# Kernel optimization log

Hardware: AMD Instinct MI355X
Metric: run time of the kernel (lower is better)

Reference implementation:

```python
import jax, jax.numpy as jnp
import numpy as np

N = 100000   # nodes
E = 1600000  # edges (before self loops)
IN, HID, OUT = 128, 128, 64


def setup_inputs() -> dict:
    key = jax.random.key(0)
    ks = jax.random.split(key, 5)
    x = jax.random.normal(ks[0], (N, IN), dtype=jnp.float32)
    edge_index = jax.random.randint(ks[1], (2, E), 0, N, dtype=jnp.int32)
    W1 = jax.random.normal(ks[2], (IN, HID), dtype=jnp.float32) * (1.0 / np.sqrt(IN))
    b1 = jnp.zeros((HID,), dtype=jnp.float32)
    W2 = jax.random.normal(ks[3], (HID, OUT), dtype=jnp.float32) * (1.0 / np.sqrt(HID))
    b2 = jnp.zeros((OUT,), dtype=jnp.float32)
    return {"x": x, "edge_index": edge_index, "W1": W1, "b1": b1, "W2": W2, "b2": b2}


def _gcn_conv(x, W, b, src, dst, norm):
    # linear transform first (small GEMM), then normalized scatter-add aggregation
    h = x @ W                                   # [N, d_out]
    msg = h[src] * norm[:, None]                # [E+N, d_out] gathered messages
    agg = jax.ops.segment_sum(msg, dst, num_segments=N)
    return agg + b


def reference(x, edge_index, W1, b1, W2, b2):
    loops = jnp.arange(N, dtype=edge_index.dtype)
    src = jnp.concatenate([edge_index[0], loops])   # add self loops (PyG GCNConv default)
    dst = jnp.concatenate([edge_index[1], loops])
    # symmetric normalization D^{-1/2} (A+I) D^{-1/2}
    deg = jax.ops.segment_sum(jnp.ones_like(dst, dtype=x.dtype), dst, num_segments=N)
    dinv = jnp.where(deg > 0, jax.lax.rsqrt(deg), 0.0)
    norm = dinv[src] * dinv[dst]                # [E+N]

    h = _gcn_conv(x, W1, b1, src, dst, norm)
    h = jax.nn.relu(h)
    out = _gcn_conv(h, W2, b2, src, dst, norm)
    return out
```

## Files before the change

kernel.cpp:

```cpp
#include <hip/hip_runtime.h>
#include <hip/hip_bf16.h>

#define IN_DIM  128
#define HID_DIM 128
#define OUT_DIM 64
#define NREP    8

typedef unsigned short ushort_t;
struct ushort4_t { ushort_t x, y, z, w; };
typedef __attribute__((ext_vector_type(8))) short bf16x8;
typedef __attribute__((ext_vector_type(4))) float f32x4;

__device__ __forceinline__ float bf2f(ushort_t u) {
    return __uint_as_float(((unsigned int)u) << 16);
}
__device__ __forceinline__ short f2bf_s(float v) {
    __hip_bfloat16 t = __float2bfloat16(v);
    return *(short*)&t;
}
__device__ __forceinline__ unsigned int pack2(float a, float b) {
    return ((unsigned int)(ushort_t)f2bf_s(b) << 16) | (ushort_t)f2bf_s(a);
}

__global__ void count_rank(const int* __restrict__ dst, int E, int N,
                           int* __restrict__ cntR, int* __restrict__ rank) {
    int e = blockIdx.x * blockDim.x + threadIdx.x;
    if (e < E) {
        int r = (e >> 8) & (NREP - 1);
        rank[e] = atomicAdd(&cntR[(size_t)r * N + dst[e]], 1);
    }
}

__global__ void node_totals(int* __restrict__ cntR, float* __restrict__ dinv,
                            int* __restrict__ cntp, int* __restrict__ bsum, int N) {
    __shared__ int wsum[4];
    const int t = threadIdx.x;
    const int base = blockIdx.x * 2048 + t * 8;
    int ssum = 0;
    #pragma unroll
    for (int i = 0; i < 8; ++i) {
        const int idx = base + i;
        if (idx < N) {
            int b = 0;
            #pragma unroll
            for (int r = 0; r < NREP; ++r) {
                int c = cntR[(size_t)r * N + idx];
                cntR[(size_t)r * N + idx] = b;
                b += c;
            }
            dinv[idx] = rsqrtf((float)(b + 1));
            int p = (b + 7) & ~7;
            cntp[idx] = p;
            ssum += p;
        }
    }
    #pragma unroll
    for (int off = 32; off > 0; off >>= 1) ssum += __shfl_down(ssum, off);
    const int lane = t & 63, w = t >> 6;
    if (lane == 0) wsum[w] = ssum;
    __syncthreads();
    if (t == 0) bsum[blockIdx.x] = wsum[0] + wsum[1] + wsum[2] + wsum[3];
}

__global__ void scan_partials(int* __restrict__ bsum, int S) {
    const int t = threadIdx.x;
    int running = 0;
    for (int base = 0; base < S; base += 64) {
        int i = base + t;
        int v = (i < S) ? bsum[i] : 0;
        int incl = v;
        #pragma unroll
        for (int off = 1; off < 64; off <<= 1) {
            int u = __shfl_up(incl, off);
            if (t >= off) incl += u;
        }
        if (i < S) bsum[i] = running + incl - v;
        running += __shfl(incl, 63);
    }
}

__global__ void scan_write(const int* __restrict__ cntp, const int* __restrict__ bsum,
                           int* __restrict__ row_start, int N) {
    __shared__ int wsum[4];
    const int t = threadIdx.x;
    const int base = blockIdx.x * 2048 + t * 8;
    int v[8];
    #pragma unroll
    for (int i = 0; i < 8; ++i) v[i] = (base + i < N) ? cntp[base + i] : 0;
    int s = v[0] + v[1] + v[2] + v[3] + v[4] + v[5] + v[6] + v[7];
    const int lane = t & 63, w = t >> 6;
    int incl = s;
    #pragma unroll
    for (int off = 1; off < 64; off <<= 1) {
        int u = __shfl_up(incl, off);
        if (lane >= off) incl += u;
    }
    if (lane == 63) wsum[w] = incl;
    __syncthreads();
    int woff = 0;
    for (int i = 0; i < w; ++i) woff += wsum[i];
    int run = bsum[blockIdx.x] + woff + (incl - s);
    #pragma unroll
    for (int i = 0; i < 8; ++i) {
        if (base + i < N) row_start[base + i] = run;
        run += v[i];
    }
}

__global__ void fill_pack(const int* __restrict__ src, const int* __restrict__ dst,
                          const int* __restrict__ rank, const int* __restrict__ row_start,
                          const int* __restrict__ cntR, const float* __restrict__ dinv,
                          int E, int N, int2* __restrict__ pack) {
    int e = blockIdx.x * blockDim.x + threadIdx.x;
    if (e < E) {
        int s = src[e], d = dst[e];
        int r = (e >> 8) & (NREP - 1);
        int pos = row_start[d] + cntR[(size_t)r * N + d] + rank[e];
        int2 p;
        p.x = s;
        p.y = __float_as_int(dinv[s] * dinv[d]);
        pack[pos] = p;
    }
}

__global__ __launch_bounds__(256, 2) void gemm1_mfma(
        const float* __restrict__ x, const float* __restrict__ W,
        unsigned int* __restrict__ h, int N, int NT, int NW) {
    const int tid  = threadIdx.x;
    const int lane = tid & 63;
    const int m    = lane & 15;
    const int quad = lane >> 4;
    const int gw   = blockIdx.x * 4 + (tid >> 6);

    bf16x8 a[8][4];
    #pragma unroll
    for (int ct = 0; ct < 8; ++ct)
        #pragma unroll
        for (int kc = 0; kc < 4; ++kc)
            #pragma unroll
            for (int j = 0; j < 8; ++j)
                a[ct][kc][j] = f2bf_s(W[(size_t)(kc * 32 + quad * 8 + j) * HID_DIM + ct * 16 + m]);

    for (int t = gw; t < NT; t += NW) {
        const int n0 = t * 16;
        int node = n0 + m; if (node >= N) node = N - 1;
        const float* xr = x + (size_t)node * IN_DIM + quad * 8;
        f32x4 acc[8];
        #pragma unroll
        for (int ct = 0; ct < 8; ++ct) acc[ct] = (f32x4){0.f, 0.f, 0.f, 0.f};
        #pragma unroll
        for (int kc = 0; kc < 4; ++kc) {
            const float4 v0 = *(const float4*)(xr + kc * 32);
            const float4 v1 = *(const float4*)(xr + kc * 32 + 4);
            bf16x8 b;
            b[0] = f2bf_s(v0.x); b[1] = f2bf_s(v0.y); b[2] = f2bf_s(v0.z); b[3] = f2bf_s(v0.w);
            b[4] = f2bf_s(v1.x); b[5] = f2bf_s(v1.y); b[6] = f2bf_s(v1.z); b[7] = f2bf_s(v1.w);
            #pragma unroll
            for (int ct = 0; ct < 8; ++ct)
                acc[ct] = __builtin_amdgcn_mfma_f32_16x16x32_bf16(a[ct][kc], b, acc[ct], 0, 0, 0);
        }
        if (n0 + m < N) {
            unsigned int* o = h + (size_t)(n0 + m) * (HID_DIM / 2) + quad * 2;
            #pragma unroll
            for (int ct = 0; ct < 8; ++ct) {
                uint2 pv;
                pv.x = pack2(acc[ct][0], acc[ct][1]);
                pv.y = pack2(acc[ct][2], acc[ct][3]);
                *(uint2*)(o + ct * 8) = pv;
            }
        }
    }
}

__global__ __launch_bounds__(256) void gemm2_mfma(
        const ushort_t* __restrict__ agg, const float* __restrict__ b1,
        const float* __restrict__ W2, unsigned int* __restrict__ h2,
        int N, int NT, int NW) {
    const int tid  = threadIdx.x;
    const int lane = tid & 63;
    const int m    = lane & 15;
    const int quad = lane >> 4;
    const int gw   = blockIdx.x * 4 + (tid >> 6);

    bf16x8 a[4][4];
    #pragma unroll
    for (int ct = 0; ct < 4; ++ct)
        #pragma unroll
        for (int kc = 0; kc < 4; ++kc)
            #pragma unroll
            for (int j = 0; j < 8; ++j)
                a[ct][kc][j] = f2bf_s(W2[(size_t)(kc * 32 + quad * 8 + j) * OUT_DIM + ct * 16 + m]);

    float4 b1v[8];
    #pragma unroll
    for (int kc = 0; kc < 4; ++kc) {
        b1v[kc * 2]     = *(const float4*)(b1 + kc * 32 + quad * 8);
        b1v[kc * 2 + 1] = *(const float4*)(b1 + kc * 32 + quad * 8 + 4);
    }

    for (int t = gw; t < NT; t += NW) {
        const int n0 = t * 16;
        int node = n0 + m; if (node >= N) node = N - 1;
        const ushort_t* ar = agg + (size_t)node * HID_DIM + quad * 8;
        f32x4 acc[4];
        #pragma unroll
        for (int ct = 0; ct < 4; ++ct) acc[ct] = (f32x4){0.f, 0.f, 0.f, 0.f};
        #pragma unroll
        for (int kc = 0; kc < 4; ++kc) {
            const ushort4_t r0 = *(const ushort4_t*)(ar + kc * 32);
            const ushort4_t r1 = *(const ushort4_t*)(ar + kc * 32 + 4);
            const float4 ba = b1v[kc * 2], bb = b1v[kc * 2 + 1];
            bf16x8 b;
            b[0] = f2bf_s(fmaxf(bf2f(r0.x) + ba.x, 0.f));
            b[1] = f2bf_s(fmaxf(bf2f(r0.y) + ba.y, 0.f));
            b[2] = f2bf_s(fmaxf(bf2f(r0.z) + ba.z, 0.f));
            b[3] = f2bf_s(fmaxf(bf2f(r0.w) + ba.w, 0.f));
            b[4] = f2bf_s(fmaxf(bf2f(r1.x) + bb.x, 0.f));
            b[5] = f2bf_s(fmaxf(bf2f(r1.y) + bb.y, 0.f));
            b[6] = f2bf_s(fmaxf(bf2f(r1.z) + bb.z, 0.f));
            b[7] = f2bf_s(fmaxf(bf2f(r1.w) + bb.w, 0.f));
            #pragma unroll
            for (int ct = 0; ct < 4; ++ct)
                acc[ct] = __builtin_amdgcn_mfma_f32_16x16x32_bf16(a[ct][kc], b, acc[ct], 0, 0, 0);
        }
        if (n0 + m < N) {
            unsigned int* o = h2 + (size_t)(n0 + m) * (OUT_DIM / 2) + quad * 2;
            #pragma unroll
            for (int ct = 0; ct < 4; ++ct) {
                uint2 pv;
                pv.x = pack2(acc[ct][0], acc[ct][1]);
                pv.y = pack2(acc[ct][2], acc[ct][3]);
                *(uint2*)(o + ct * 8) = pv;
            }
        }
    }
}

template<int D, bool BF16_OUT>
__global__ void gather_bf16(const ushort_t* __restrict__ h, const int2* __restrict__ pack,
                            const int* __restrict__ row_start, const int* __restrict__ cntp,
                            const float* __restrict__ dinv, const float* __restrict__ bias,
                            int N, void* __restrict__ outv) {
    const int TPN = D / 4;
    const int NPB = 256 / TPN;
    const int t = threadIdx.x;
    const int node = blockIdx.x * NPB + t / TPN;
    if (node >= N) return;
    const int f = (t & (TPN - 1)) * 4;
    const float dd = dinv[node];

    const ushort4_t self = *(const ushort4_t*)(h + (size_t)node * D + f);
    const float sn = dd * dd;
    float4 acc;
    acc.x = bf2f(self.x) * sn; acc.y = bf2f(self.y) * sn;
    acc.z = bf2f(self.z) * sn; acc.w = bf2f(self.w) * sn;
    if (bias) {
        const float4 b = *(const float4*)(bias + f);
        acc.x += b.x; acc.y += b.y; acc.z += b.z; acc.w += b.w;
    }

    const int2* pk = pack + row_start[node];
    const int cpad = cntp[node];
    for (int e = 0; e < cpad; e += 8) {
        const int4 p0 = *(const int4*)(pk + e);
        const int4 p1 = *(const int4*)(pk + e + 2);
        const int4 p2 = *(const int4*)(pk + e + 4);
        const int4 p3 = *(const int4*)(pk + e + 6);
        int   si[8];
        float ni[8];
        si[0] = p0.x; ni[0] = __int_as_float(p0.y);
        si[1] = p0.z; ni[1] = __int_as_float(p0.w);
        si[2] = p1.x; ni[2] = __int_as_float(p1.y);
        si[3] = p1.z; ni[3] = __int_as_float(p1.w);
        si[4] = p2.x; ni[4] = __int_as_float(p2.y);
        si[5] = p2.z; ni[5] = __int_as_float(p2.w);
        si[6] = p3.x; ni[6] = __int_as_float(p3.y);
        si[7] = p3.z; ni[7] = __int_as_float(p3.w);
        ushort4_t v[8];
        #pragma unroll
        for (int i = 0; i < 8; ++i)
            v[i] = *(const ushort4_t*)(h + (size_t)si[i] * D + f);
        #pragma unroll
        for (int i = 0; i < 8; ++i) {
            acc.x += bf2f(v[i].x) * ni[i]; acc.y += bf2f(v[i].y) * ni[i];
            acc.z += bf2f(v[i].z) * ni[i]; acc.w += bf2f(v[i].w) * ni[i];
        }
    }
    if (BF16_OUT) {
        unsigned int* out = (unsigned int*)outv;
        uint2 pv;
        pv.x = pack2(acc.x, acc.y);
        pv.y = pack2(acc.z, acc.w);
        *(uint2*)(out + ((size_t)node * D + f) / 2) = pv;
    } else {
        float* out = (float*)outv;
        *(float4*)(out + (size_t)node * D + f) = acc;
    }
}

extern "C" void kernel_launch(void* const* d_in, const int* in_sizes, int n_in,
                              void* d_out, int out_size, void* d_ws, size_t ws_size,
                              hipStream_t stream) {
    const float* x   = (const float*)d_in[0];
    const int*   ei  = (const int*)  d_in[1];
    const float* W1  = (const float*)d_in[2];
    const float* b1  = (const float*)d_in[3];
    const float* W2  = (const float*)d_in[4];
    const float* b2  = (const float*)d_in[5];
    float* out = (float*)d_out;

    const int N = in_sizes[0] / IN_DIM;
    const int E = in_sizes[1] / 2;
    const int* src = ei;
    const int* dst = ei + E;

    const int PACK_CAP = E + 8 * N;
    float* dinv      = (float*)d_ws;
    int*   cntp      = (int*)(dinv + N);
    int*   row_start = cntp + N;
    int*   bsum      = row_start + N;
    int*   cntR      = bsum + 1024;
    size_t off       = (size_t)(3 * N + 1024 + NREP * N);
    off = (off + 3) & ~(size_t)3;
    int2*  pack      = (int2*)((int*)d_ws + off);
    unsigned int* h1 = (unsigned int*)(pack + PACK_CAP);
    unsigned int* agg1 = h1 + (size_t)N * (HID_DIM / 2);
    int*   rank      = (int*)agg1;
    unsigned int* h2 = h1;

    const int B = 256;
    const int S = (N + 2047) / 2048;
    const int NT = (N + 15) / 16;

    hipMemsetAsync(cntR, 0, (size_t)NREP * N * sizeof(int), stream);
    hipMemsetAsync(pack, 0, (size_t)PACK_CAP * sizeof(int2), stream);
    count_rank<<<(E + B - 1) / B, B, 0, stream>>>(dst, E, N, cntR, rank);
    node_totals<<<S, 256, 0, stream>>>(cntR, dinv, cntp, bsum, N);
    scan_partials<<<1, 64, 0, stream>>>(bsum, S);
    scan_write<<<S, 256, 0, stream>>>(cntp, bsum, row_start, N);
    fill_pack<<<(E + B - 1) / B, B, 0, stream>>>(
        src, dst, rank, row_start, cntR, dinv, E, N, pack);

    gemm1_mfma<<<512, 256, 0, stream>>>(x, W1, h1, N, NT, 512 * 4);

    gather_bf16<HID_DIM, true><<<(N + 7) / 8, 256, 0, stream>>>(
        (const ushort_t*)h1, pack, row_start, cntp, dinv, nullptr, N, (void*)agg1);

    gemm2_mfma<<<768, 256, 0, stream>>>(
        (const ushort_t*)agg1, b1, W2, h2, N, NT, 768 * 4);

    gather_bf16<OUT_DIM, false><<<(N + 15) / 16, 256, 0, stream>>>(
        (const ushort_t*)h2, pack, row_start, cntp, dinv, b2, N, (void*)out);
}
```

Before: 354.8 us.

## Widen gather loads to 16 bytes and pick count replica by XCC id

The gather kernel now has each thread handle 8 bf16 features with 128-bit loads instead of 4 with 64-bit loads. This halves the threads per node, doubles the nodes per block, and doubles the in-flight bytes per gathered neighbor. The degree-count atomics now choose their replica from the hardware XCC id instead of the edge index, so atomics stay local to one die's L2. The replica index is packed into the top bits of the rank for fill_pack to recover. This assumes rank fits in 28 bits and relies on reading a hardware register.

```diff
diff --git a/kernel.cpp b/kernel.cpp
--- a/kernel.cpp
+++ b/kernel.cpp
@@ -21,13 +21,21 @@
 __device__ __forceinline__ unsigned int pack2(float a, float b) {
     return ((unsigned int)(ushort_t)f2bf_s(b) << 16) | (ushort_t)f2bf_s(a);
 }
+__device__ __forceinline__ void bf2x(unsigned int u, float& lo, float& hi) {
+    lo = __uint_as_float(u << 16);
+    hi = __uint_as_float(u & 0xffff0000u);
+}
+__device__ __forceinline__ int xcc_id() {
+    return __builtin_amdgcn_s_getreg((3 << 11) | (0 << 6) | 20) & (NREP - 1);
+}
 
 __global__ void count_rank(const int* __restrict__ dst, int E, int N,
                            int* __restrict__ cntR, int* __restrict__ rank) {
     int e = blockIdx.x * blockDim.x + threadIdx.x;
     if (e < E) {
-        int r = (e >> 8) & (NREP - 1);
-        rank[e] = atomicAdd(&cntR[(size_t)r * N + dst[e]], 1);
+        int r = xcc_id();
+        int rk = atomicAdd(&cntR[(size_t)r * N + dst[e]], 1);
+        rank[e] = (r << 28) | rk;
     }
 }
 
@@ -114,8 +122,10 @@
     int e = blockIdx.x * blockDim.x + threadIdx.x;
     if (e < E) {
         int s = src[e], d = dst[e];
-        int r = (e >> 8) & (NREP - 1);
-        int pos = row_start[d] + cntR[(size_t)r * N + d] + rank[e];
+        int rr = rank[e];
+        int r  = (unsigned int)rr >> 28;
+        int rk = rr & 0x0FFFFFFF;
+        int pos = row_start[d] + cntR[(size_t)r * N + d] + rk;
         int2 p;
         p.x = s;
         p.y = __float_as_int(dinv[s] * dinv[d]);
@@ -241,22 +251,29 @@
                             const int* __restrict__ row_start, const int* __restrict__ cntp,
                             const float* __restrict__ dinv, const float* __restrict__ bias,
                             int N, void* __restrict__ outv) {
-    const int TPN = D / 4;
+    const int TPN = D / 8;
     const int NPB = 256 / TPN;
     const int t = threadIdx.x;
     const int node = blockIdx.x * NPB + t / TPN;
     if (node >= N) return;
-    const int f = (t & (TPN - 1)) * 4;
+    const int f = (t & (TPN - 1)) * 8;
     const float dd = dinv[node];
 
-    const ushort4_t self = *(const ushort4_t*)(h + (size_t)node * D + f);
-    const float sn = dd * dd;
-    float4 acc;
-    acc.x = bf2f(self.x) * sn; acc.y = bf2f(self.y) * sn;
-    acc.z = bf2f(self.z) * sn; acc.w = bf2f(self.w) * sn;
+    float acc[8];
+    {
+        const uint4 su = *(const uint4*)(h + (size_t)node * D + f);
+        const float sn = dd * dd;
+        float l, hi2;
+        bf2x(su.x, l, hi2); acc[0] = l * sn; acc[1] = hi2 * sn;
+        bf2x(su.y, l, hi2); acc[2] = l * sn; acc[3] = hi2 * sn;
+        bf2x(su.z, l, hi2); acc[4] = l * sn; acc[5] = hi2 * sn;
+        bf2x(su.w, l, hi2); acc[6] = l * sn; acc[7] = hi2 * sn;
+    }
     if (bias) {
-        const float4 b = *(const float4*)(bias + f);
-        acc.x += b.x; acc.y += b.y; acc.z += b.z; acc.w += b.w;
+        const float4 b0 = *(const float4*)(bias + f);
+        const float4 b1 = *(const float4*)(bias + f + 4);
+        acc[0] += b0.x; acc[1] += b0.y; acc[2] += b0.z; acc[3] += b0.w;
+        acc[4] += b1.x; acc[5] += b1.y; acc[6] += b1.z; acc[7] += b1.w;
     }
 
     const int2* pk = pack + row_start[node];
@@ -276,25 +293,33 @@
         si[5] = p2.z; ni[5] = __int_as_float(p2.w);
         si[6] = p3.x; ni[6] = __int_as_float(p3.y);
         si[7] = p3.z; ni[7] = __int_as_float(p3.w);
-        ushort4_t v[8];
+        uint4 v[8];
         #pragma unroll
         for (int i = 0; i < 8; ++i)
-            v[i] = *(const ushort4_t*)(h + (size_t)si[i] * D + f);
+            v[i] = *(const uint4*)(h + (size_t)si[i] * D + f);
         #pragma unroll
         for (int i = 0; i < 8; ++i) {
-            acc.x += bf2f(v[i].x) * ni[i]; acc.y += bf2f(v[i].y) * ni[i];
-            acc.z += bf2f(v[i].z) * ni[i]; acc.w += bf2f(v[i].w) * ni[i];
+            float l, hi2;
+            bf2x(v[i].x, l, hi2); acc[0] += l * ni[i]; acc[1] += hi2 * ni[i];
+            bf2x(v[i].y, l, hi2); acc[2] += l * ni[i]; acc[3] += hi2 * ni[i];
+            bf2x(v[i].z, l, hi2); acc[4] += l * ni[i]; acc[5] += hi2 * ni[i];
+            bf2x(v[i].w, l, hi2); acc[6] += l * ni[i]; acc[7] += hi2 * ni[i];
         }
     }
     if (BF16_OUT) {
         unsigned int* out = (unsigned int*)outv;
-        uint2 pv;
-        pv.x = pack2(acc.x, acc.y);
-        pv.y = pack2(acc.z, acc.w);
-        *(uint2*)(out + ((size_t)node * D + f) / 2) = pv;
+        uint4 pv;
+        pv.x = pack2(acc[0], acc[1]);
+        pv.y = pack2(acc[2], acc[3]);
+        pv.z = pack2(acc[4], acc[5]);
+        pv.w = pack2(acc[6], acc[7]);
+        *(uint4*)(out + ((size_t)node * D + f) / 2) = pv;
     } else {
         float* out = (float*)outv;
-        *(float4*)(out + (size_t)node * D + f) = acc;
+        float4 o0 = {acc[0], acc[1], acc[2], acc[3]};
+        float4 o1 = {acc[4], acc[5], acc[6], acc[7]};
+        *(float4*)(out + (size_t)node * D + f)     = o0;
+        *(float4*)(out + (size_t)node * D + f + 4) = o1;
     }
 }
 
@@ -343,12 +368,12 @@
 
     gemm1_mfma<<<512, 256, 0, stream>>>(x, W1, h1, N, NT, 512 * 4);
 
-    gather_bf16<HID_DIM, true><<<(N + 7) / 8, 256, 0, stream>>>(
+    gather_bf16<HID_DIM, true><<<(N + 15) / 16, 256, 0, stream>>>(
         (const ushort_t*)h1, pack, row_start, cntp, dinv, nullptr, N, (void*)agg1);
 
     gemm2_mfma<<<768, 256, 0, stream>>>(
         (const ushort_t*)agg1, b1, W2, h2, N, NT, 768 * 4);
 
-    gather_bf16<OUT_DIM, false><<<(N + 15) / 16, 256, 0, stream>>>(
+    gather_bf16<OUT_DIM, false><<<(N + 31) / 32, 256, 0, stream>>>(
         (const ushort_t*)h2, pack, row_start, cntp, dinv, b2, N, (void*)out);
 }
```

Result: no change. 349.4 us (-1.5%).
